# Kernel optimization log

Hardware: AMD Instinct MI355X
Metric: run time of the kernel (lower is better)

Reference implementation:

```python
import jax, jax.numpy as jnp
import numpy as np

N = 1048576   # total nodes
E = 8388608   # total edges
IN = 5        # in_channels
H = 32        # hid_channels
G = 16384     # num graphs
C = 10        # num_classes
L = 2         # conv_unit
EPS = 1e-5


def setup_inputs() -> dict:
    key = jax.random.key(0)
    ks = jax.random.split(key, 16)
    x = jax.random.normal(ks[0], (N, IN), dtype=jnp.float32)
    edge_index = jax.random.randint(ks[1], (2, E), 0, N, dtype=jnp.int64)
    edge_attr = jax.random.uniform(ks[2], (E, 1), dtype=jnp.float32)
    batch = jnp.sort(jax.random.randint(ks[3], (N,), 0, G, dtype=jnp.int64))
    s_in = 1.0 / np.sqrt(IN)
    s_h = 1.0 / np.sqrt(H)
    s_2h = 1.0 / np.sqrt(2 * H)
    W_emb = jax.random.normal(ks[4], (H, IN), dtype=jnp.float32) * s_in
    b_emb = jnp.zeros((H,), dtype=jnp.float32)
    W_rel = jax.random.normal(ks[5], (L, H, H), dtype=jnp.float32) * s_h
    b_rel = jnp.zeros((L, H), dtype=jnp.float32)
    W_root = jax.random.normal(ks[6], (L, H, H), dtype=jnp.float32) * s_h
    bn_gamma = jnp.ones((L, H), dtype=jnp.float32)
    bn_beta = jnp.zeros((L, H), dtype=jnp.float32)
    W1 = jax.random.normal(ks[7], (2 * H, H), dtype=jnp.float32) * s_h
    b1 = jnp.zeros((2 * H,), dtype=jnp.float32)
    W2 = jax.random.normal(ks[8], (C, 2 * H), dtype=jnp.float32) * s_2h
    b2 = jnp.zeros((C,), dtype=jnp.float32)
    return {
        "x": x, "edge_index": edge_index, "edge_attr": edge_attr, "batch": batch,
        "W_emb": W_emb, "b_emb": b_emb, "W_rel": W_rel, "b_rel": b_rel,
        "W_root": W_root, "bn_gamma": bn_gamma, "bn_beta": bn_beta,
        "W1": W1, "b1": b1, "W2": W2, "b2": b2,
    }


def _graph_conv(x, src, dst, ew, Wrel, brel, Wroot):
    # PyG GraphConv: lin_rel(scatter_add(ew * x[src] -> dst)) + lin_root(x)
    msg = x[src] * ew[:, None]                              # [E, H]
    agg = jax.ops.segment_sum(msg, dst, num_segments=N)     # [N, H]
    return agg @ Wrel.T + brel + x @ Wroot.T


def _batch_norm(x, gamma, beta):
    mean = jnp.mean(x, axis=0)
    var = jnp.mean(jnp.square(x - mean), axis=0)  # biased, as torch training BN
    return (x - mean) * jax.lax.rsqrt(var + EPS) * gamma + beta


def reference(x, edge_index, edge_attr, batch, W_emb, b_emb, W_rel, b_rel,
              W_root, bn_gamma, bn_beta, W1, b1, W2, b2):
    src, dst = edge_index[0], edge_index[1]
    ew = edge_attr.reshape(-1)
    h = x @ W_emb.T + b_emb                                  # node_emb
    for i in range(L):
        h = _graph_conv(h, src, dst, ew, W_rel[i], b_rel[i], W_root[i])
        h = jax.nn.relu(_batch_norm(h, bn_gamma[i], bn_beta[i]))
    graph_x = jax.ops.segment_max(h, batch, num_segments=G)  # global_max_pool
    hidden = jax.nn.relu(graph_x @ W1.T + b1)
    return hidden @ W2.T + b2                                # [G, C]
```

## Files before the change

### kernel.cpp

```cpp
#include <hip/hip_runtime.h>
#include <hip/hip_fp16.h>

#define NN 1048576
#define NE 8388608
#define NG 16384
#define NBUCK 1024
#define BSH 10
#define PBLK 256
#define EPB (NE / PBLK)

typedef _Float16 half8 __attribute__((ext_vector_type(8)));
typedef float f32x16 __attribute__((ext_vector_type(16)));

__global__ __launch_bounds__(256) void k_embed(const float* __restrict__ x,
    const float* __restrict__ W, const float* __restrict__ b, __half* __restrict__ h) {
  __shared__ float sW[160];
  __shared__ float sb[32];
  int t = threadIdx.x;
  if (t < 160) sW[t] = W[t];
  if (t < 32) sb[t] = b[t];
  __syncthreads();
  int idx = blockIdx.x * 256 + t;
  int c = idx & 31, n = idx >> 5;
  const float* xr = x + n * 5;
  float acc = sb[c];
#pragma unroll
  for (int k = 0; k < 5; ++k) acc = fmaf(xr[k], sW[c * 5 + k], acc);
  h[idx] = __float2half(acc);
}

__global__ __launch_bounds__(256) void k_pcnt(const int* __restrict__ dst, int* __restrict__ hist) {
  __shared__ int lh[NBUCK];
  int t = threadIdx.x;
#pragma unroll
  for (int k = 0; k < 4; ++k) lh[t + k * 256] = 0;
  __syncthreads();
  int base = blockIdx.x * EPB;
  for (int e = base + t; e < base + EPB; e += 256)
    atomicAdd(&lh[dst[e] >> BSH], 1);
  __syncthreads();
#pragma unroll
  for (int k = 0; k < 4; ++k) {
    int b = t + k * 256;
    hist[b * PBLK + blockIdx.x] = lh[b];
  }
}

__global__ __launch_bounds__(256) void k_scanA(int* __restrict__ hist, int* __restrict__ tot) {
  __shared__ int s2[256];
  int b = blockIdx.x, t = threadIdx.x;
  int v = hist[b * PBLK + t];
  s2[t] = v; __syncthreads();
  for (int st = 1; st < 256; st <<= 1) {
    int a = (t >= st) ? s2[t - st] : 0; __syncthreads(); s2[t] += a; __syncthreads();
  }
  hist[b * PBLK + t] = s2[t] - v;
  if (t == 255) tot[b] = s2[255];
}

__global__ __launch_bounds__(256) void k_scanB(const int* __restrict__ tot, int* __restrict__ gbase) {
  __shared__ int s2[256];
  int t = threadIdx.x;
  int v0 = tot[4 * t], v1 = tot[4 * t + 1], v2 = tot[4 * t + 2], v3 = tot[4 * t + 3];
  int tsum = v0 + v1 + v2 + v3;
  s2[t] = tsum; __syncthreads();
  for (int st = 1; st < 256; st <<= 1) {
    int a = (t >= st) ? s2[t - st] : 0; __syncthreads(); s2[t] += a; __syncthreads();
  }
  int ex = s2[t] - tsum;
  gbase[4 * t] = ex;
  gbase[4 * t + 1] = ex + v0;
  gbase[4 * t + 2] = ex + v0 + v1;
  gbase[4 * t + 3] = ex + v0 + v1 + v2;
  if (t == 255) gbase[NBUCK] = ex + tsum;
}

__global__ __launch_bounds__(256) void k_part(const int* __restrict__ ei, const float* __restrict__ ew,
                                              const int* __restrict__ hist, const int* __restrict__ gbase,
                                              uint2* __restrict__ bsw) {
  __shared__ int cur[NBUCK];
  int t = threadIdx.x, blk = blockIdx.x;
#pragma unroll
  for (int k = 0; k < 4; ++k) {
    int b = t + k * 256;
    cur[b] = gbase[b] + hist[b * PBLK + blk];
  }
  __syncthreads();
  int base = blk * EPB;
  for (int e = base + t; e < base + EPB; e += 256) {
    int src = ei[e];
    int d   = ei[NE + e];
    unsigned wb = __float_as_uint(ew[e]);
    int b = d >> BSH;
    int pos = atomicAdd(&cur[b], 1);
    bsw[pos] = make_uint2(((unsigned)src << BSH) | (unsigned)(d & (NBUCK - 1)), wb);
  }
}

__global__ __launch_bounds__(256) void k_fillD(const int* __restrict__ gbase, const uint2* __restrict__ bsw,
                                               int* __restrict__ rowptr, uint2* __restrict__ colw) {
  __shared__ int loc[NBUCK];
  __shared__ int s2[256];
  int t = threadIdx.x, b = blockIdx.x;
  int beg = gbase[b], end = gbase[b + 1], gb = beg;
  int node_base = b << BSH;
#pragma unroll
  for (int j = 0; j < 4; ++j) loc[t * 4 + j] = 0;
  __syncthreads();
  for (int i = beg + t; i < end; i += 256) atomicAdd(&loc[bsw[i].x & (NBUCK - 1)], 1);
  __syncthreads();
  int v[4]; int tsum = 0;
#pragma unroll
  for (int j = 0; j < 4; ++j) { v[j] = loc[t * 4 + j]; tsum += v[j]; }
  s2[t] = tsum; __syncthreads();
  for (int st = 1; st < 256; st <<= 1) {
    int a = (t >= st) ? s2[t - st] : 0; __syncthreads(); s2[t] += a; __syncthreads();
  }
  int run = s2[t] - tsum;
#pragma unroll
  for (int j = 0; j < 4; ++j) {
    loc[t * 4 + j] = run;
    rowptr[node_base + t * 4 + j] = gb + run;
    run += v[j];
  }
  if (b == NBUCK - 1 && t == 255) rowptr[NN] = NE;
  __syncthreads();
  for (int i = beg + t; i < end; i += 256) {
    uint2 r = bsw[i];
    int p = atomicAdd(&loc[r.x & (NBUCK - 1)], 1);
    colw[gb + p] = make_uint2(r.x >> BSH, r.y);
  }
}

__global__ __launch_bounds__(256) void k_gbound(const int* __restrict__ batch, int* __restrict__ gptr) {
  int n = blockIdx.x * 256 + threadIdx.x;
  int b = batch[n];
  int prev = (n == 0) ? -1 : batch[n - 1];
  for (int g = prev + 1; g <= b; ++g) gptr[g] = n;
  if (n == NN - 1) {
    for (int g = b + 1; g <= NG; ++g) gptr[g] = NN;
  }
}

__global__ __launch_bounds__(256) void k_agglin(
    const int* __restrict__ rowptr, const uint2* __restrict__ colw,
    const __half* __restrict__ hIn, const float* __restrict__ Wrel,
    const float* __restrict__ brel, const float* __restrict__ Wroot,
    __half* __restrict__ hPre, double* __restrict__ stats) {
  __shared__ __half sA[4][1024];
  __shared__ uint2 sE[256];
  __shared__ double rS[256], rQ[256];
  int t = threadIdx.x;
  int wv = t >> 6, lane = t & 63;
  int c = lane & 31, hi = lane >> 5, grp = t >> 5;
  char* myA = (char*)sA[wv];

  half8 bfr[4];
#pragma unroll
  for (int m = 0; m < 4; ++m)
#pragma unroll
    for (int j = 0; j < 8; ++j) {
      int k = 16 * m + hi * 8 + j;
      float w = (k < 32) ? Wrel[c * 32 + k] : Wroot[c * 32 + (k - 32)];
      bfr[m][j] = (_Float16)w;
    }
  float bias = brel[c];
  double aS = 0.0, aQ = 0.0;

  for (int tile = blockIdx.x * 4 + wv; tile < NN / 32; tile += gridDim.x * 4) {
    int nbase = tile * 32;
    for (int r = 0; r < 16; ++r) {
      int node = 2 * r + hi;
      int n = nbase + node;
      int r0 = rowptr[n], r1 = rowptr[n + 1];
      float acc = 0.f;
      for (int j = r0; j < r1; j += 32) {
        int m_ = r1 - j; if (m_ > 32) m_ = 32;
        uint2 cw = make_uint2(0u, 0u);
        if (c < m_) cw = colw[j + c];
        sE[t] = cw;
        int mm = (m_ + 7) & ~7;
        for (int i = 0; i < mm; i += 8) {
          const uint4* eb4 = (const uint4*)&sE[grp * 32 + i];
          uint4 q0 = eb4[0], q1 = eb4[1], q2 = eb4[2], q3 = eb4[3];
          float h0 = __half2float(hIn[(size_t)q0.x * 32 + c]);
          float h1 = __half2float(hIn[(size_t)q0.z * 32 + c]);
          float h2 = __half2float(hIn[(size_t)q1.x * 32 + c]);
          float h3 = __half2float(hIn[(size_t)q1.z * 32 + c]);
          float h4 = __half2float(hIn[(size_t)q2.x * 32 + c]);
          float h5 = __half2float(hIn[(size_t)q2.z * 32 + c]);
          float h6 = __half2float(hIn[(size_t)q3.x * 32 + c]);
          float h7 = __half2float(hIn[(size_t)q3.z * 32 + c]);
          acc = fmaf(__uint_as_float(q0.y), h0, acc);
          acc = fmaf(__uint_as_float(q0.w), h1, acc);
          acc = fmaf(__uint_as_float(q1.y), h2, acc);
          acc = fmaf(__uint_as_float(q1.w), h3, acc);
          acc = fmaf(__uint_as_float(q2.y), h4, acc);
          acc = fmaf(__uint_as_float(q2.w), h5, acc);
          acc = fmaf(__uint_as_float(q3.y), h6, acc);
          acc = fmaf(__uint_as_float(q3.w), h7, acc);
        }
      }
      int bw = (node * 64 + c * 2) ^ ((node & 7) << 4);
      *(__half*)(myA + bw) = __float2half(acc);
    }
    f32x16 d;
#pragma unroll
    for (int r = 0; r < 16; ++r) d[r] = bias;
#pragma unroll
    for (int m = 0; m < 4; ++m) {
      half8 a;
      if (m < 2) {
        int node = c;
        int br = (node * 64 + (16 * m + hi * 8) * 2) ^ ((node & 7) << 4);
        a = *(const half8*)(myA + br);
      } else {
        int chb = 16 * (m - 2) + hi * 8;
        a = *(const half8*)(hIn + (size_t)(nbase + c) * 32 + chb);
      }
      d = __builtin_amdgcn_mfma_f32_32x32x16_f16(a, bfr[m], d, 0, 0, 0);
    }
#pragma unroll
    for (int r = 0; r < 16; ++r) {
      int node = (r & 3) + 8 * (r >> 2) + 4 * hi;
      float v = d[r];
      hPre[(size_t)(nbase + node) * 32 + c] = __float2half(v);
      aS += v; aQ += (double)v * v;
    }
  }
  rS[t] = aS; rQ[t] = aQ;
  __syncthreads();
  for (int s = 128; s >= 32; s >>= 1) {
    if (t < s) { rS[t] += rS[t + s]; rQ[t] += rQ[t + s]; }
    __syncthreads();
  }
  if (t < 32) {
    atomicAdd(&stats[t], rS[t]);
    atomicAdd(&stats[32 + t], rQ[t]);
  }
}

__global__ void k_bnfin(const double* __restrict__ stats, const float* __restrict__ gamma,
                        const float* __restrict__ beta, float* __restrict__ ss) {
  int c = threadIdx.x;
  double mean = stats[c] * (1.0 / NN);
  double var = stats[32 + c] * (1.0 / NN) - mean * mean;
  float scale = gamma[c] * (float)(1.0 / sqrt(var + 1e-5));
  ss[c] = scale;
  ss[32 + c] = beta[c] - (float)mean * scale;
}

__global__ __launch_bounds__(256) void k_apply(const __half* __restrict__ in,
    const float* __restrict__ ss, __half* __restrict__ outp) {
  __shared__ float s0[32], s1[32];
  int t = threadIdx.x;
  if (t < 32) { s0[t] = ss[t]; s1[t] = ss[32 + t]; }
  __syncthreads();
  int idx = blockIdx.x * 256 + t;
  int c = idx & 31;
  float v = fmaxf(fmaf(__half2float(in[idx]), s0[c], s1[c]), 0.f);
  outp[idx] = __float2half(v);
}

__global__ __launch_bounds__(256) void k_pool(const __half* __restrict__ hB,
    const float* __restrict__ ss, const int* __restrict__ gptr, float* __restrict__ pooled) {
  int t = threadIdx.x;
  int wv = t >> 6, lane = t & 63;
  int p = lane >> 4, cl = lane & 15;
  float s0x = ss[2 * cl], s0y = ss[2 * cl + 1];
  float s1x = ss[32 + 2 * cl], s1y = ss[32 + 2 * cl + 1];
  int g = blockIdx.x * 4 + wv;
  int a = gptr[g], b = gptr[g + 1];
  float mx = 0.f, my = 0.f;
  for (int n = a + p; n < b; n += 4) {
    float2 hv = __half22float2(*(const __half2*)(hB + (size_t)n * 32 + 2 * cl));
    mx = fmaxf(mx, fmaf(hv.x, s0x, s1x));
    my = fmaxf(my, fmaf(hv.y, s0y, s1y));
  }
  mx = fmaxf(mx, __shfl_xor(mx, 16, 64)); my = fmaxf(my, __shfl_xor(my, 16, 64));
  mx = fmaxf(mx, __shfl_xor(mx, 32, 64)); my = fmaxf(my, __shfl_xor(my, 32, 64));
  if (p == 0) *(float2*)&pooled[g * 32 + 2 * cl] = make_float2(mx, my);
}

__global__ __launch_bounds__(256) void k_head(const float* __restrict__ pooled,
    const float* __restrict__ W1, const float* __restrict__ b1,
    const float* __restrict__ W2, const float* __restrict__ b2, float* __restrict__ out) {
  __shared__ float sW1[64 * 33], sW2[10 * 65], sb1[64], sb2[10];
  __shared__ float sHid[4][64];
  int t = threadIdx.x;
  for (int i = t; i < 2048; i += 256) sW1[(i >> 5) * 33 + (i & 31)] = W1[i];
  for (int i = t; i < 640; i += 256) sW2[(i >> 6) * 65 + (i & 63)] = W2[i];
  if (t < 64) sb1[t] = b1[t];
  if (t < 10) sb2[t] = b2[t];
  __syncthreads();
  int w = t >> 6, lane = t & 63;
  for (int g = blockIdx.x * 4 + w; g < NG; g += gridDim.x * 4) {
    float pv = (lane < 32) ? pooled[g * 32 + lane] : 0.f;
    float acc = sb1[lane];
#pragma unroll
    for (int k = 0; k < 32; ++k)
      acc = fmaf(__shfl(pv, k, 64), sW1[lane * 33 + k], acc);
    acc = fmaxf(acc, 0.f);
    sHid[w][lane] = acc;
    __syncthreads();
    if (lane < 10) {
      float o = sb2[lane];
#pragma unroll
      for (int j = 0; j < 64; ++j) o = fmaf(sHid[w][j], sW2[lane * 65 + j], o);
      out[g * 10 + lane] = o;
    }
    __syncthreads();
  }
}

extern "C" void kernel_launch(void* const* d_in, const int* in_sizes, int n_in,
                              void* d_out, int out_size, void* d_ws, size_t ws_size,
                              hipStream_t stream) {
  const float* x      = (const float*)d_in[0];
  const int*   ei     = (const int*)d_in[1];
  const float* ea     = (const float*)d_in[2];
  const int*   batch  = (const int*)d_in[3];
  const float* W_emb  = (const float*)d_in[4];
  const float* b_emb  = (const float*)d_in[5];
  const float* W_rel  = (const float*)d_in[6];
  const float* b_rel  = (const float*)d_in[7];
  const float* W_root = (const float*)d_in[8];
  const float* gamma  = (const float*)d_in[9];
  const float* beta   = (const float*)d_in[10];
  const float* W1     = (const float*)d_in[11];
  const float* b1     = (const float*)d_in[12];
  const float* W2     = (const float*)d_in[13];
  const float* b2     = (const float*)d_in[14];
  float* out = (float*)d_out;

  char* ws = (char*)d_ws;
  size_t off = 0;
  __half* hA    = (__half*)(ws + off); off += (size_t)NN * 32 * 2;
  uint2*  colw  = (uint2*)(ws + off);  off += (size_t)NE * 8;
  uint2*  bsw   = (uint2*)(ws + off);
  __half* hB    = (__half*)(ws + off);
  off += (size_t)NE * 8;
  int*    rowptr= (int*)(ws + off);    off += ((size_t)NN + 64) * 4;
  int*    hist  = (int*)(ws + off);    off += (size_t)NBUCK * PBLK * 4;
  int*    tot   = (int*)(ws + off);    off += NBUCK * 4;
  int*    gbase = (int*)(ws + off);    off += (NBUCK + 64) * 4;
  int*    gptr  = (int*)(ws + off);    off += ((size_t)NG + 64) * 4;
  float*  pooled= (float*)(ws + off);
  double* stats = (double*)d_out;
  float*  ss0   = (float*)((char*)d_out + 512);
  float*  ss1   = (float*)((char*)d_out + 768);

  k_embed<<<NN * 32 / 256, 256, 0, stream>>>(x, W_emb, b_emb, hA);

  k_pcnt <<<PBLK, 256, 0, stream>>>(ei + NE, hist);
  k_scanA<<<NBUCK, 256, 0, stream>>>(hist, tot);
  k_scanB<<<1, 256, 0, stream>>>(tot, gbase);
  k_part <<<PBLK, 256, 0, stream>>>(ei, ea, hist, gbase, bsw);
  k_fillD<<<NBUCK, 256, 0, stream>>>(gbase, bsw, rowptr, colw);
  k_gbound<<<NN / 256, 256, 0, stream>>>(batch, gptr);

  (void)hipMemsetAsync(stats, 0, 64 * 8, stream);
  k_agglin<<<2048, 256, 0, stream>>>(rowptr, colw, hA, W_rel, b_rel, W_root, hB, stats);
  k_bnfin<<<1, 32, 0, stream>>>(stats, gamma, beta, ss0);
  k_apply<<<NN * 32 / 256, 256, 0, stream>>>(hB, ss0, hA);

  (void)hipMemsetAsync(stats, 0, 64 * 8, stream);
  k_agglin<<<2048, 256, 0, stream>>>(rowptr, colw, hA, W_rel + 1024, b_rel + 32,
                                     W_root + 1024, hB, stats);
  k_bnfin<<<1, 32, 0, stream>>>(stats, gamma + 32, beta + 32, ss1);

  k_pool<<<NG / 4, 256, 0, stream>>>(hB, ss1, gptr, pooled);
  k_head<<<1024, 256, 0, stream>>>(pooled, W1, b1, W2, b2, out);
}
```

Before: 1.023 ms.

## Replace full CSR build with bucketed edges and LDS atomic aggregation

Drops the second-level per-node sort (k_fillD) and the CSR rowptr/colw arrays. Edges are instead partitioned into 4096 buckets of 256 destination nodes, and each aggregation block accumulates messages into a shared-memory float tile with LDS atomics before the MFMA linear step. This removes one full pass over the edge array and the per-node irregular row loop, at the cost of LDS atomic contention and a larger shared footprint (about 33 KB) that may limit occupancy. BN statistics are now accumulated per thread in float and only converted to double for the block reduction.

```diff
diff --git a/kernel.cpp b/kernel.cpp
--- a/kernel.cpp
+++ b/kernel.cpp
@@ -4,9 +4,9 @@
 #define NN 1048576
 #define NE 8388608
 #define NG 16384
-#define NBUCK 1024
-#define BSH 10
-#define PBLK 256
+#define NBUCK 4096
+#define BSH 8
+#define PBLK 128
 #define EPB (NE / PBLK)
 
 typedef _Float16 half8 __attribute__((ext_vector_type(8)));
@@ -33,46 +33,45 @@
   __shared__ int lh[NBUCK];
   int t = threadIdx.x;
 #pragma unroll
-  for (int k = 0; k < 4; ++k) lh[t + k * 256] = 0;
+  for (int k = 0; k < 16; ++k) lh[t + k * 256] = 0;
   __syncthreads();
   int base = blockIdx.x * EPB;
   for (int e = base + t; e < base + EPB; e += 256)
     atomicAdd(&lh[dst[e] >> BSH], 1);
   __syncthreads();
 #pragma unroll
-  for (int k = 0; k < 4; ++k) {
+  for (int k = 0; k < 16; ++k) {
     int b = t + k * 256;
     hist[b * PBLK + blockIdx.x] = lh[b];
   }
 }
 
-__global__ __launch_bounds__(256) void k_scanA(int* __restrict__ hist, int* __restrict__ tot) {
-  __shared__ int s2[256];
+__global__ __launch_bounds__(128) void k_scanA(int* __restrict__ hist, int* __restrict__ tot) {
+  __shared__ int s2[128];
   int b = blockIdx.x, t = threadIdx.x;
   int v = hist[b * PBLK + t];
   s2[t] = v; __syncthreads();
-  for (int st = 1; st < 256; st <<= 1) {
+  for (int st = 1; st < 128; st <<= 1) {
     int a = (t >= st) ? s2[t - st] : 0; __syncthreads(); s2[t] += a; __syncthreads();
   }
   hist[b * PBLK + t] = s2[t] - v;
-  if (t == 255) tot[b] = s2[255];
+  if (t == 127) tot[b] = s2[127];
 }
 
 __global__ __launch_bounds__(256) void k_scanB(const int* __restrict__ tot, int* __restrict__ gbase) {
   __shared__ int s2[256];
   int t = threadIdx.x;
-  int v0 = tot[4 * t], v1 = tot[4 * t + 1], v2 = tot[4 * t + 2], v3 = tot[4 * t + 3];
-  int tsum = v0 + v1 + v2 + v3;
+  int v[16]; int tsum = 0;
+#pragma unroll
+  for (int j = 0; j < 16; ++j) { v[j] = tot[t * 16 + j]; tsum += v[j]; }
   s2[t] = tsum; __syncthreads();
   for (int st = 1; st < 256; st <<= 1) {
     int a = (t >= st) ? s2[t - st] : 0; __syncthreads(); s2[t] += a; __syncthreads();
   }
   int ex = s2[t] - tsum;
-  gbase[4 * t] = ex;
-  gbase[4 * t + 1] = ex + v0;
-  gbase[4 * t + 2] = ex + v0 + v1;
-  gbase[4 * t + 3] = ex + v0 + v1 + v2;
-  if (t == 255) gbase[NBUCK] = ex + tsum;
+#pragma unroll
+  for (int j = 0; j < 16; ++j) { gbase[t * 16 + j] = ex; ex += v[j]; }
+  if (t == 255) gbase[NBUCK] = ex;
 }
 
 __global__ __launch_bounds__(256) void k_part(const int* __restrict__ ei, const float* __restrict__ ew,
@@ -81,7 +80,7 @@
   __shared__ int cur[NBUCK];
   int t = threadIdx.x, blk = blockIdx.x;
 #pragma unroll
-  for (int k = 0; k < 4; ++k) {
+  for (int k = 0; k < 16; ++k) {
     int b = t + k * 256;
     cur[b] = gbase[b] + hist[b * PBLK + blk];
   }
@@ -93,42 +92,7 @@
     unsigned wb = __float_as_uint(ew[e]);
     int b = d >> BSH;
     int pos = atomicAdd(&cur[b], 1);
-    bsw[pos] = make_uint2(((unsigned)src << BSH) | (unsigned)(d & (NBUCK - 1)), wb);
-  }
-}
-
-__global__ __launch_bounds__(256) void k_fillD(const int* __restrict__ gbase, const uint2* __restrict__ bsw,
-                                               int* __restrict__ rowptr, uint2* __restrict__ colw) {
-  __shared__ int loc[NBUCK];
-  __shared__ int s2[256];
-  int t = threadIdx.x, b = blockIdx.x;
-  int beg = gbase[b], end = gbase[b + 1], gb = beg;
-  int node_base = b << BSH;
-#pragma unroll
-  for (int j = 0; j < 4; ++j) loc[t * 4 + j] = 0;
-  __syncthreads();
-  for (int i = beg + t; i < end; i += 256) atomicAdd(&loc[bsw[i].x & (NBUCK - 1)], 1);
-  __syncthreads();
-  int v[4]; int tsum = 0;
-#pragma unroll
-  for (int j = 0; j < 4; ++j) { v[j] = loc[t * 4 + j]; tsum += v[j]; }
-  s2[t] = tsum; __syncthreads();
-  for (int st = 1; st < 256; st <<= 1) {
-    int a = (t >= st) ? s2[t - st] : 0; __syncthreads(); s2[t] += a; __syncthreads();
-  }
-  int run = s2[t] - tsum;
-#pragma unroll
-  for (int j = 0; j < 4; ++j) {
-    loc[t * 4 + j] = run;
-    rowptr[node_base + t * 4 + j] = gb + run;
-    run += v[j];
-  }
-  if (b == NBUCK - 1 && t == 255) rowptr[NN] = NE;
-  __syncthreads();
-  for (int i = beg + t; i < end; i += 256) {
-    uint2 r = bsw[i];
-    int p = atomicAdd(&loc[r.x & (NBUCK - 1)], 1);
-    colw[gb + p] = make_uint2(r.x >> BSH, r.y);
+    bsw[pos] = make_uint2(((unsigned)src << BSH) | (unsigned)(d & 255), wb);
   }
 }
 
@@ -143,17 +107,18 @@
 }
 
 __global__ __launch_bounds__(256) void k_agglin(
-    const int* __restrict__ rowptr, const uint2* __restrict__ colw,
+    const int* __restrict__ gbase, const uint2* __restrict__ bsw,
     const __half* __restrict__ hIn, const float* __restrict__ Wrel,
     const float* __restrict__ brel, const float* __restrict__ Wroot,
     __half* __restrict__ hPre, double* __restrict__ stats) {
-  __shared__ __half sA[4][1024];
+  __shared__ float agg[256 * 33];
   __shared__ uint2 sE[256];
   __shared__ double rS[256], rQ[256];
   int t = threadIdx.x;
   int wv = t >> 6, lane = t & 63;
   int c = lane & 31, hi = lane >> 5, grp = t >> 5;
-  char* myA = (char*)sA[wv];
+  int b = blockIdx.x;
+  int beg = gbase[b], end = gbase[b + 1];
 
   half8 bfr[4];
 #pragma unroll
@@ -165,45 +130,44 @@
       bfr[m][j] = (_Float16)w;
     }
   float bias = brel[c];
-  double aS = 0.0, aQ = 0.0;
-
-  for (int tile = blockIdx.x * 4 + wv; tile < NN / 32; tile += gridDim.x * 4) {
-    int nbase = tile * 32;
-    for (int r = 0; r < 16; ++r) {
-      int node = 2 * r + hi;
-      int n = nbase + node;
-      int r0 = rowptr[n], r1 = rowptr[n + 1];
-      float acc = 0.f;
-      for (int j = r0; j < r1; j += 32) {
-        int m_ = r1 - j; if (m_ > 32) m_ = 32;
-        uint2 cw = make_uint2(0u, 0u);
-        if (c < m_) cw = colw[j + c];
-        sE[t] = cw;
-        int mm = (m_ + 7) & ~7;
-        for (int i = 0; i < mm; i += 8) {
-          const uint4* eb4 = (const uint4*)&sE[grp * 32 + i];
-          uint4 q0 = eb4[0], q1 = eb4[1], q2 = eb4[2], q3 = eb4[3];
-          float h0 = __half2float(hIn[(size_t)q0.x * 32 + c]);
-          float h1 = __half2float(hIn[(size_t)q0.z * 32 + c]);
-          float h2 = __half2float(hIn[(size_t)q1.x * 32 + c]);
-          float h3 = __half2float(hIn[(size_t)q1.z * 32 + c]);
-          float h4 = __half2float(hIn[(size_t)q2.x * 32 + c]);
-          float h5 = __half2float(hIn[(size_t)q2.z * 32 + c]);
-          float h6 = __half2float(hIn[(size_t)q3.x * 32 + c]);
-          float h7 = __half2float(hIn[(size_t)q3.z * 32 + c]);
-          acc = fmaf(__uint_as_float(q0.y), h0, acc);
-          acc = fmaf(__uint_as_float(q0.w), h1, acc);
-          acc = fmaf(__uint_as_float(q1.y), h2, acc);
-          acc = fmaf(__uint_as_float(q1.w), h3, acc);
-          acc = fmaf(__uint_as_float(q2.y), h4, acc);
-          acc = fmaf(__uint_as_float(q2.w), h5, acc);
-          acc = fmaf(__uint_as_float(q3.y), h6, acc);
-          acc = fmaf(__uint_as_float(q3.w), h7, acc);
-        }
-      }
-      int bw = (node * 64 + c * 2) ^ ((node & 7) << 4);
-      *(__half*)(myA + bw) = __float2half(acc);
-    }
+
+  for (int i = t; i < 256 * 33; i += 256) agg[i] = 0.f;
+  __syncthreads();
+
+  for (int j0 = beg + grp * 32; j0 < end; j0 += 8 * 32) {
+    int m_ = end - j0; if (m_ > 32) m_ = 32;
+    uint2 cw = make_uint2(0u, 0u);
+    if (c < m_) cw = bsw[j0 + c];
+    sE[t] = cw;
+    int mm = (m_ + 7) & ~7;
+    for (int i = 0; i < mm; i += 8) {
+      const uint4* eb4 = (const uint4*)&sE[grp * 32 + i];
+      uint4 q0 = eb4[0], q1 = eb4[1], q2 = eb4[2], q3 = eb4[3];
+      float h0 = __half2float(hIn[(size_t)(q0.x >> BSH) * 32 + c]);
+      float h1 = __half2float(hIn[(size_t)(q0.z >> BSH) * 32 + c]);
+      float h2 = __half2float(hIn[(size_t)(q1.x >> BSH) * 32 + c]);
+      float h3 = __half2float(hIn[(size_t)(q1.z >> BSH) * 32 + c]);
+      float h4 = __half2float(hIn[(size_t)(q2.x >> BSH) * 32 + c]);
+      float h5 = __half2float(hIn[(size_t)(q2.z >> BSH) * 32 + c]);
+      float h6 = __half2float(hIn[(size_t)(q3.x >> BSH) * 32 + c]);
+      float h7 = __half2float(hIn[(size_t)(q3.z >> BSH) * 32 + c]);
+      atomicAdd(&agg[(q0.x & 255) * 33 + c], __uint_as_float(q0.y) * h0);
+      atomicAdd(&agg[(q0.z & 255) * 33 + c], __uint_as_float(q0.w) * h1);
+      atomicAdd(&agg[(q1.x & 255) * 33 + c], __uint_as_float(q1.y) * h2);
+      atomicAdd(&agg[(q1.z & 255) * 33 + c], __uint_as_float(q1.w) * h3);
+      atomicAdd(&agg[(q2.x & 255) * 33 + c], __uint_as_float(q2.y) * h4);
+      atomicAdd(&agg[(q2.z & 255) * 33 + c], __uint_as_float(q2.w) * h5);
+      atomicAdd(&agg[(q3.x & 255) * 33 + c], __uint_as_float(q3.y) * h6);
+      atomicAdd(&agg[(q3.z & 255) * 33 + c], __uint_as_float(q3.w) * h7);
+    }
+  }
+  __syncthreads();
+
+  float aS = 0.f, aQ = 0.f;
+#pragma unroll
+  for (int tt = 0; tt < 2; ++tt) {
+    int nloc = (wv * 2 + tt) * 32;
+    int nglob = b * 256 + nloc;
     f32x16 d;
 #pragma unroll
     for (int r = 0; r < 16; ++r) d[r] = bias;
@@ -211,12 +175,12 @@
     for (int m = 0; m < 4; ++m) {
       half8 a;
       if (m < 2) {
-        int node = c;
-        int br = (node * 64 + (16 * m + hi * 8) * 2) ^ ((node & 7) << 4);
-        a = *(const half8*)(myA + br);
+        const float* row = &agg[(nloc + c) * 33 + 16 * m + hi * 8];
+#pragma unroll
+        for (int j = 0; j < 8; ++j) a[j] = (_Float16)row[j];
       } else {
         int chb = 16 * (m - 2) + hi * 8;
-        a = *(const half8*)(hIn + (size_t)(nbase + c) * 32 + chb);
+        a = *(const half8*)(hIn + (size_t)(nglob + c) * 32 + chb);
       }
       d = __builtin_amdgcn_mfma_f32_32x32x16_f16(a, bfr[m], d, 0, 0, 0);
     }
@@ -224,11 +188,11 @@
     for (int r = 0; r < 16; ++r) {
       int node = (r & 3) + 8 * (r >> 2) + 4 * hi;
       float v = d[r];
-      hPre[(size_t)(nbase + node) * 32 + c] = __float2half(v);
-      aS += v; aQ += (double)v * v;
-    }
-  }
-  rS[t] = aS; rQ[t] = aQ;
+      hPre[(size_t)(nglob + node) * 32 + c] = __float2half(v);
+      aS += v; aQ += v * v;
+    }
+  }
+  rS[t] = (double)aS; rQ[t] = (double)aQ;
   __syncthreads();
   for (int s = 128; s >= 32; s >>= 1) {
     if (t < s) { rS[t] += rS[t + s]; rQ[t] += rQ[t + s]; }
@@ -336,11 +300,8 @@
   char* ws = (char*)d_ws;
   size_t off = 0;
   __half* hA    = (__half*)(ws + off); off += (size_t)NN * 32 * 2;
-  uint2*  colw  = (uint2*)(ws + off);  off += (size_t)NE * 8;
-  uint2*  bsw   = (uint2*)(ws + off);
-  __half* hB    = (__half*)(ws + off);
-  off += (size_t)NE * 8;
-  int*    rowptr= (int*)(ws + off);    off += ((size_t)NN + 64) * 4;
+  __half* hB    = (__half*)(ws + off); off += (size_t)NN * 32 * 2;
+  uint2*  bsw   = (uint2*)(ws + off);  off += (size_t)NE * 8;
   int*    hist  = (int*)(ws + off);    off += (size_t)NBUCK * PBLK * 4;
   int*    tot   = (int*)(ws + off);    off += NBUCK * 4;
   int*    gbase = (int*)(ws + off);    off += (NBUCK + 64) * 4;
@@ -353,20 +314,19 @@
   k_embed<<<NN * 32 / 256, 256, 0, stream>>>(x, W_emb, b_emb, hA);
 
   k_pcnt <<<PBLK, 256, 0, stream>>>(ei + NE, hist);
-  k_scanA<<<NBUCK, 256, 0, stream>>>(hist, tot);
+  k_scanA<<<NBUCK, 128, 0, stream>>>(hist, tot);
   k_scanB<<<1, 256, 0, stream>>>(tot, gbase);
   k_part <<<PBLK, 256, 0, stream>>>(ei, ea, hist, gbase, bsw);
-  k_fillD<<<NBUCK, 256, 0, stream>>>(gbase, bsw, rowptr, colw);
   k_gbound<<<NN / 256, 256, 0, stream>>>(batch, gptr);
 
   (void)hipMemsetAsync(stats, 0, 64 * 8, stream);
-  k_agglin<<<2048, 256, 0, stream>>>(rowptr, colw, hA, W_rel, b_rel, W_root, hB, stats);
+  k_agglin<<<NBUCK, 256, 0, stream>>>(gbase, bsw, hA, W_rel, b_rel, W_root, hB, stats);
   k_bnfin<<<1, 32, 0, stream>>>(stats, gamma, beta, ss0);
   k_apply<<<NN * 32 / 256, 256, 0, stream>>>(hB, ss0, hA);
 
   (void)hipMemsetAsync(stats, 0, 64 * 8, stream);
-  k_agglin<<<2048, 256, 0, stream>>>(rowptr, colw, hA, W_rel + 1024, b_rel + 32,
-                                     W_root + 1024, hB, stats);
+  k_agglin<<<NBUCK, 256, 0, stream>>>(gbase, bsw, hA, W_rel + 1024, b_rel + 32,
+                                      W_root + 1024, hB, stats);
   k_bnfin<<<1, 32, 0, stream>>>(stats, gamma + 32, beta + 32, ss1);
 
   k_pool<<<NG / 4, 256, 0, stream>>>(hB, ss1, gptr, pooled);
```

After: 3.347 ms. 3.27x slower.

## Use finer CSR buckets and stage bucket records in shared memory

Applied to the files above, without the earlier changes.

The CSR build now partitions edges into 4096 buckets of 256 nodes using 128 partition blocks, instead of 1024 buckets of 1024 nodes with 256 blocks. The second-pass fill kernel copies each bucket's records into shared memory once, up to a capacity of 2600 records, then does the counting and scatter passes from there, so global memory is read once instead of twice. Oversized buckets fall back to global reads. In exchange there are more histogram entries per partition block and larger shared memory use, which may reduce occupancy.

```diff
diff --git a/kernel.cpp b/kernel.cpp
--- a/kernel.cpp
+++ b/kernel.cpp
@@ -4,10 +4,11 @@
 #define NN 1048576
 #define NE 8388608
 #define NG 16384
-#define NBUCK 1024
-#define BSH 10
-#define PBLK 256
+#define NBUCK 4096
+#define BSH 8
+#define PBLK 128
 #define EPB (NE / PBLK)
+#define SCAP 2600
 
 typedef _Float16 half8 __attribute__((ext_vector_type(8)));
 typedef float f32x16 __attribute__((ext_vector_type(16)));
@@ -33,46 +34,45 @@
   __shared__ int lh[NBUCK];
   int t = threadIdx.x;
 #pragma unroll
-  for (int k = 0; k < 4; ++k) lh[t + k * 256] = 0;
+  for (int k = 0; k < 16; ++k) lh[t + k * 256] = 0;
   __syncthreads();
   int base = blockIdx.x * EPB;
   for (int e = base + t; e < base + EPB; e += 256)
     atomicAdd(&lh[dst[e] >> BSH], 1);
   __syncthreads();
 #pragma unroll
-  for (int k = 0; k < 4; ++k) {
+  for (int k = 0; k < 16; ++k) {
     int b = t + k * 256;
     hist[b * PBLK + blockIdx.x] = lh[b];
   }
 }
 
-__global__ __launch_bounds__(256) void k_scanA(int* __restrict__ hist, int* __restrict__ tot) {
-  __shared__ int s2[256];
+__global__ __launch_bounds__(128) void k_scanA(int* __restrict__ hist, int* __restrict__ tot) {
+  __shared__ int s2[128];
   int b = blockIdx.x, t = threadIdx.x;
   int v = hist[b * PBLK + t];
   s2[t] = v; __syncthreads();
-  for (int st = 1; st < 256; st <<= 1) {
+  for (int st = 1; st < 128; st <<= 1) {
     int a = (t >= st) ? s2[t - st] : 0; __syncthreads(); s2[t] += a; __syncthreads();
   }
   hist[b * PBLK + t] = s2[t] - v;
-  if (t == 255) tot[b] = s2[255];
+  if (t == 127) tot[b] = s2[127];
 }
 
 __global__ __launch_bounds__(256) void k_scanB(const int* __restrict__ tot, int* __restrict__ gbase) {
   __shared__ int s2[256];
   int t = threadIdx.x;
-  int v0 = tot[4 * t], v1 = tot[4 * t + 1], v2 = tot[4 * t + 2], v3 = tot[4 * t + 3];
-  int tsum = v0 + v1 + v2 + v3;
+  int v[16]; int tsum = 0;
+#pragma unroll
+  for (int j = 0; j < 16; ++j) { v[j] = tot[t * 16 + j]; tsum += v[j]; }
   s2[t] = tsum; __syncthreads();
   for (int st = 1; st < 256; st <<= 1) {
     int a = (t >= st) ? s2[t - st] : 0; __syncthreads(); s2[t] += a; __syncthreads();
   }
   int ex = s2[t] - tsum;
-  gbase[4 * t] = ex;
-  gbase[4 * t + 1] = ex + v0;
-  gbase[4 * t + 2] = ex + v0 + v1;
-  gbase[4 * t + 3] = ex + v0 + v1 + v2;
-  if (t == 255) gbase[NBUCK] = ex + tsum;
+#pragma unroll
+  for (int j = 0; j < 16; ++j) { gbase[t * 16 + j] = ex; ex += v[j]; }
+  if (t == 255) gbase[NBUCK] = ex;
 }
 
 __global__ __launch_bounds__(256) void k_part(const int* __restrict__ ei, const float* __restrict__ ew,
@@ -81,7 +81,7 @@
   __shared__ int cur[NBUCK];
   int t = threadIdx.x, blk = blockIdx.x;
 #pragma unroll
-  for (int k = 0; k < 4; ++k) {
+  for (int k = 0; k < 16; ++k) {
     int b = t + k * 256;
     cur[b] = gbase[b] + hist[b * PBLK + blk];
   }
@@ -93,41 +93,42 @@
     unsigned wb = __float_as_uint(ew[e]);
     int b = d >> BSH;
     int pos = atomicAdd(&cur[b], 1);
-    bsw[pos] = make_uint2(((unsigned)src << BSH) | (unsigned)(d & (NBUCK - 1)), wb);
-  }
-}
-
-__global__ __launch_bounds__(256) void k_fillD(const int* __restrict__ gbase, const uint2* __restrict__ bsw,
-                                               int* __restrict__ rowptr, uint2* __restrict__ colw) {
-  __shared__ int loc[NBUCK];
+    bsw[pos] = make_uint2(((unsigned)src << BSH) | (unsigned)(d & 255), wb);
+  }
+}
+
+__global__ __launch_bounds__(256) void k_fillD2(const int* __restrict__ gbase, const uint2* __restrict__ bsw,
+                                                int* __restrict__ rowptr, uint2* __restrict__ colw) {
+  __shared__ uint2 rec[SCAP];
+  __shared__ int loc[256];
   __shared__ int s2[256];
   int t = threadIdx.x, b = blockIdx.x;
   int beg = gbase[b], end = gbase[b + 1], gb = beg;
-  int node_base = b << BSH;
-#pragma unroll
-  for (int j = 0; j < 4; ++j) loc[t * 4 + j] = 0;
-  __syncthreads();
-  for (int i = beg + t; i < end; i += 256) atomicAdd(&loc[bsw[i].x & (NBUCK - 1)], 1);
-  __syncthreads();
-  int v[4]; int tsum = 0;
-#pragma unroll
-  for (int j = 0; j < 4; ++j) { v[j] = loc[t * 4 + j]; tsum += v[j]; }
-  s2[t] = tsum; __syncthreads();
+  int cnt = end - beg;
+  bool staged = (cnt <= SCAP);
+  loc[t] = 0;
+  if (staged) {
+    for (int i = t; i < cnt; i += 256) rec[i] = bsw[beg + i];
+  }
+  __syncthreads();
+  for (int i = t; i < cnt; i += 256) {
+    unsigned rx = staged ? rec[i].x : bsw[beg + i].x;
+    atomicAdd(&loc[rx & 255], 1);
+  }
+  __syncthreads();
+  int v = loc[t];
+  s2[t] = v; __syncthreads();
   for (int st = 1; st < 256; st <<= 1) {
     int a = (t >= st) ? s2[t - st] : 0; __syncthreads(); s2[t] += a; __syncthreads();
   }
-  int run = s2[t] - tsum;
-#pragma unroll
-  for (int j = 0; j < 4; ++j) {
-    loc[t * 4 + j] = run;
-    rowptr[node_base + t * 4 + j] = gb + run;
-    run += v[j];
-  }
+  int base_t = s2[t] - v;
+  rowptr[(b << BSH) + t] = gb + base_t;
+  loc[t] = base_t;
   if (b == NBUCK - 1 && t == 255) rowptr[NN] = NE;
   __syncthreads();
-  for (int i = beg + t; i < end; i += 256) {
-    uint2 r = bsw[i];
-    int p = atomicAdd(&loc[r.x & (NBUCK - 1)], 1);
+  for (int i = t; i < cnt; i += 256) {
+    uint2 r = staged ? rec[i] : bsw[beg + i];
+    int p = atomicAdd(&loc[r.x & 255], 1);
     colw[gb + p] = make_uint2(r.x >> BSH, r.y);
   }
 }
@@ -353,10 +354,10 @@
   k_embed<<<NN * 32 / 256, 256, 0, stream>>>(x, W_emb, b_emb, hA);
 
   k_pcnt <<<PBLK, 256, 0, stream>>>(ei + NE, hist);
-  k_scanA<<<NBUCK, 256, 0, stream>>>(hist, tot);
+  k_scanA<<<NBUCK, 128, 0, stream>>>(hist, tot);
   k_scanB<<<1, 256, 0, stream>>>(tot, gbase);
   k_part <<<PBLK, 256, 0, stream>>>(ei, ea, hist, gbase, bsw);
-  k_fillD<<<NBUCK, 256, 0, stream>>>(gbase, bsw, rowptr, colw);
+  k_fillD2<<<NBUCK, 256, 0, stream>>>(gbase, bsw, rowptr, colw);
   k_gbound<<<NN / 256, 256, 0, stream>>>(batch, gptr);
 
   (void)hipMemsetAsync(stats, 0, 64 * 8, stream);
```

Result: slower. 1.115 ms (+9.0%).
